# Optimization experiments

Hardware: AMD Instinct MI355X
Metric: run time of the kernel (lower is better)

Reference implementation:

```python
import jax, jax.numpy as jnp
import numpy as np

B, T, D = 2, 2048, 1280
H = 20
DH = D // H  # 64
S_PAST = 2048


def setup_inputs() -> dict:
    key = jax.random.key(0)
    ks = jax.random.split(key, 7)
    return {
        "x": jax.random.normal(ks[0], (B, T, D), dtype=jnp.float32),
        "past_K": jax.random.normal(ks[1], (B, H, S_PAST, DH), dtype=jnp.float32),
        "past_V": jax.random.normal(ks[2], (B, H, S_PAST, DH), dtype=jnp.float32),
        "w_q": jax.random.normal(ks[3], (D, D), dtype=jnp.float32),
        "w_k": jax.random.normal(ks[4], (D, D), dtype=jnp.float32),
        "w_v": jax.random.normal(ks[5], (D, D), dtype=jnp.float32),
        "W_o": jax.random.normal(ks[6], (D, D), dtype=jnp.float32),
    }


def reference(x, past_K, past_V, w_q, w_k, w_v, W_o):
    b, t, _ = x.shape
    # projections
    q = x @ w_q  # [B,T,D]
    k = x @ w_k
    v = x @ w_v
    # split heads -> [B,H,T,DH]
    Q = q.reshape(b, t, H, DH).transpose(0, 2, 1, 3)
    K = k.reshape(b, t, H, DH).transpose(0, 2, 1, 3)
    V = v.reshape(b, t, H, DH).transpose(0, 2, 1, 3)
    # concat KV cache along sequence dim
    K = jnp.concatenate([past_K, K], axis=-2)  # [B,H,S_past+T,DH]
    V = jnp.concatenate([past_V, V], axis=-2)
    # attention (no causal mask, matching the original module)
    scores = jnp.einsum("bhtd,bhsd->bhts", Q, K) / jnp.sqrt(jnp.float32(DH))
    attn = jax.nn.softmax(scores, axis=-1)
    values = jnp.einsum("bhts,bhsd->bhtd", attn, V)  # [B,H,T,DH]
    values = values.transpose(0, 2, 1, 3).reshape(b, t, D)
    out = values @ W_o
    return out, K, V
```

## Files before the change

### kernel.cpp

```cpp
#include <hip/hip_runtime.h>

#define NB 2
#define NH 20
#define TT 2048
#define DD 1280
#define DHH 64
#define SP 2048
#define SS 4096
#define MM (NB*TT)

typedef __attribute__((ext_vector_type(8))) short bf16x8;
typedef __attribute__((ext_vector_type(4))) float f32x4;
typedef unsigned short u16;
typedef unsigned int u32;

__device__ __forceinline__ f32x4 mfma16(bf16x8 a, bf16x8 b, f32x4 c) {
  return __builtin_amdgcn_mfma_f32_16x16x32_bf16(a, b, c, 0, 0, 0);
}

__device__ __forceinline__ u16 f2bf(float f) {
  u32 x = __builtin_bit_cast(u32, f);
  x += 0x7fffu + ((x >> 16) & 1u);
  return (u16)(x >> 16);
}
__device__ __forceinline__ float bf2f(u16 u) {
  u32 x = ((u32)u) << 16;
  return __builtin_bit_cast(float, x);
}

__device__ __forceinline__ float fexp2(float x) {
#if __has_builtin(__builtin_amdgcn_exp2f)
  return __builtin_amdgcn_exp2f(x);
#else
  return exp2f(x);
#endif
}

__device__ __forceinline__ u32 cvtpk(float lo, float hi) {
  u32 r;
  asm("v_cvt_pk_bf16_f32 %0, %1, %2" : "=v"(r) : "v"(lo), "v"(hi));
  return r;
}

#define VMCNT0() asm volatile("s_waitcnt vmcnt(0)" ::: "memory")
#define BAR() __builtin_amdgcn_s_barrier()

template<int ROWS>
__device__ __forceinline__ void stage_swz(char* lds, const u16* __restrict__ gsrc,
                                          int ld, int tid) {
  constexpr int ITER = ROWS * 8 / 256;
#pragma unroll
  for (int i = 0; i < ITER; ++i) {
    int id = i * 256 + tid;
    int row = id >> 3, c = id & 7;
    int cs = c ^ (row & 7);
    const u16* src = gsrc + row * ld + cs * 8;
    __builtin_amdgcn_global_load_lds(
        (const __attribute__((address_space(1))) u32*)src,
        (__attribute__((address_space(3))) u32*)(lds + id * 16), 16, 0, 0);
  }
}

__device__ __forceinline__ void gload16(const u16* src, char* ldst) {
  __builtin_amdgcn_global_load_lds(
      (const __attribute__((address_space(1))) u32*)src,
      (__attribute__((address_space(3))) u32*)ldst, 16, 0, 0);
}

__device__ __forceinline__ bf16x8 frag_swz(const char* lds, int row, int cc) {
  return *(const bf16x8*)(lds + row * 128 + ((cc ^ (row & 7)) << 4));
}
__device__ __forceinline__ bf16x8 frag32(const char* lds, int row, int cc) {
  return *(const bf16x8*)(lds + row * 64 + ((cc ^ (row & 3)) << 4));
}

__global__ void splitx(const float* __restrict__ x, u16* __restrict__ xh,
                       u16* __restrict__ xl) {
  int i = blockIdx.x * 256 + threadIdx.x;
  float4 v = ((const float4*)x)[i];
  ushort4 hi, lo;
  hi.x = f2bf(v.x); lo.x = f2bf(v.x - bf2f(hi.x));
  hi.y = f2bf(v.y); lo.y = f2bf(v.y - bf2f(hi.y));
  hi.z = f2bf(v.z); lo.z = f2bf(v.z - bf2f(hi.z));
  hi.w = f2bf(v.w); lo.w = f2bf(v.w - bf2f(hi.w));
  ((ushort4*)xh)[i] = hi;
  ((ushort4*)xl)[i] = lo;
}

__global__ void transw(const float* __restrict__ wq, const float* __restrict__ wk,
                       const float* __restrict__ wv, const float* __restrict__ wo,
                       u16* __restrict__ wqkvh, u16* __restrict__ wqkvl,
                       u16* __restrict__ wot) {
  __shared__ float tile[64][65];
  int mat = blockIdx.z;
  const float* src = mat == 0 ? wq : mat == 1 ? wk : mat == 2 ? wv : wo;
  int k0 = blockIdx.x * 64, n0 = blockIdx.y * 64;
  int tid = threadIdx.x;
#pragma unroll
  for (int rep = 0; rep < 16; ++rep) {
    int id = rep * 256 + tid;
    int kl = id >> 6, nl = id & 63;
    tile[nl][kl] = src[(k0 + kl) * DD + n0 + nl];
  }
  __syncthreads();
#pragma unroll
  for (int rep = 0; rep < 16; ++rep) {
    int id = rep * 256 + tid;
    int nl = id >> 6, kl = id & 63;
    float v = tile[nl][kl];
    u16 hi = f2bf(v);
    if (mat < 3) {
      int idx = (mat * DD + n0 + nl) * DD + k0 + kl;
      wqkvh[idx] = hi;
      wqkvl[idx] = f2bf(v - bf2f(hi));
    } else {
      wot[(n0 + nl) * DD + k0 + kl] = hi;
    }
  }
}

__global__ void pastk(const float* __restrict__ pK, float* __restrict__ dK,
                      u16* __restrict__ Kh, u16* __restrict__ Kl) {
  int i = blockIdx.x * 256 + threadIdx.x;
  int e = i * 4;
  int dh = e & 63;
  int s = (e >> 6) & (SP - 1);
  int bh = e >> 17;
  float4 v = *(const float4*)(pK + e);
  int o = (bh * SS + s) * DHH + dh;
  *(float4*)(dK + o) = v;
  ushort4 hi, lo;
  hi.x = f2bf(v.x); lo.x = f2bf(v.x - bf2f(hi.x));
  hi.y = f2bf(v.y); lo.y = f2bf(v.y - bf2f(hi.y));
  hi.z = f2bf(v.z); lo.z = f2bf(v.z - bf2f(hi.z));
  hi.w = f2bf(v.w); lo.w = f2bf(v.w - bf2f(hi.w));
  *(ushort4*)(Kh + o) = hi;
  *(ushort4*)(Kl + o) = lo;
}

__global__ void pastv(const float* __restrict__ pV, float* __restrict__ dV,
                      u16* __restrict__ Vt) {
  __shared__ u16 tile[64][72];
  int bi = blockIdx.x;
  int bh = bi >> 5, st = bi & 31;
  int s0 = st * 64;
  int tid = threadIdx.x;
  const float* src = pV + (bh * SP + s0) * DHH;
  float* dst = dV + (bh * SS + s0) * DHH;
#pragma unroll
  for (int rep = 0; rep < 16; ++rep) {
    int id = rep * 256 + tid;
    int sl = id >> 6, dh = id & 63;
    float v = src[sl * DHH + dh];
    dst[sl * DHH + dh] = v;
    tile[dh][sl] = f2bf(v);
  }
  __syncthreads();
  u16* vdst = Vt + (bh * DHH) * SS + s0;
#pragma unroll
  for (int rep = 0; rep < 4; ++rep) {
    int id = rep * 256 + tid;
    int dh = id >> 4, s4 = (id & 15) * 4;
    ushort4 vv;
    vv.x = tile[dh][s4];     vv.y = tile[dh][s4 + 1];
    vv.z = tile[dh][s4 + 2]; vv.w = tile[dh][s4 + 3];
    *(ushort4*)(vdst + dh * SS + s4) = vv;
  }
}

__launch_bounds__(256, 2)
__global__ void gemm_qkv(const u16* __restrict__ xh, const u16* __restrict__ xl,
                         const u16* __restrict__ wh, const u16* __restrict__ wl,
                         u16* __restrict__ Qh, u16* __restrict__ Ql,
                         u16* __restrict__ Kh, u16* __restrict__ Kl,
                         u16* __restrict__ Vt,
                         float* __restrict__ dK, float* __restrict__ dV) {
  __shared__ __align__(16) char sm[65536];
  int tid = threadIdx.x, lane = tid & 63, w = tid >> 6;
  int wm = w >> 1, wn = w & 1;
  int r15 = lane & 15, grp = lane >> 4;
  int mBase = blockIdx.x * 128;
  int by = blockIdx.y;
  int nGlob = by * 128;
  const bool split = (by < 20);
  f32x4 acc[4][4] = {};
  int id0 = tid, id1 = 256 + tid;
  int r0 = id0 >> 2, c0 = id0 & 3;
  int r1 = id1 >> 2, c1 = id1 & 3;
  int so0 = r0 * DD + (c0 ^ (r0 & 3)) * 8;
  int so1 = r1 * DD + (c1 ^ (r1 & 3)) * 8;
  const u16* aH = xh + mBase * DD;
  const u16* aL = xl + mBase * DD;
  const u16* bH = wh + nGlob * DD;
  const u16* bL = wl + nGlob * DD;
  int do0 = id0 * 16, do1 = id1 * 16;

  auto stage = [&](int buf, int k0) {
    char* b = sm + buf * 32768;
    gload16(aH + k0 + so0, b + do0);
    gload16(aH + k0 + so1, b + do1);
    gload16(bH + k0 + so0, b + 16384 + do0);
    gload16(bH + k0 + so1, b + 16384 + do1);
    if (split) {
      gload16(aL + k0 + so0, b + 8192 + do0);
      gload16(aL + k0 + so1, b + 8192 + do1);
      gload16(bL + k0 + so0, b + 24576 + do0);
      gload16(bL + k0 + so1, b + 24576 + do1);
    }
  };
  auto compute = [&](int buf) {
    const char* b = sm + buf * 32768;
    bf16x8 fah[4], fal[4], fbh[4], fbl[4];
#pragma unroll
    for (int i = 0; i < 4; ++i) {
      fah[i] = frag32(b, wm * 64 + i * 16 + r15, grp);
      fbh[i] = frag32(b + 16384, wn * 64 + i * 16 + r15, grp);
      if (split) {
        fal[i] = frag32(b + 8192, wm * 64 + i * 16 + r15, grp);
        fbl[i] = frag32(b + 24576, wn * 64 + i * 16 + r15, grp);
      }
    }
    __builtin_amdgcn_s_setprio(1);
    if (split) {
#pragma unroll
      for (int i = 0; i < 4; ++i)
#pragma unroll
        for (int j = 0; j < 4; ++j) {
          acc[i][j] = mfma16(fah[i], fbh[j], acc[i][j]);
          acc[i][j] = mfma16(fah[i], fbl[j], acc[i][j]);
          acc[i][j] = mfma16(fal[i], fbh[j], acc[i][j]);
        }
    } else {
#pragma unroll
      for (int i = 0; i < 4; ++i)
#pragma unroll
        for (int j = 0; j < 4; ++j)
          acc[i][j] = mfma16(fah[i], fbh[j], acc[i][j]);
    }
    __builtin_amdgcn_s_setprio(0);
  };

  stage(0, 0);
  VMCNT0(); BAR();
#pragma unroll 2
  for (int step = 0; step < 39; ++step) {
    stage((step + 1) & 1, (step + 1) * 32);
    compute(step & 1);
    VMCNT0(); BAR();
  }
  compute(1);

  int proj = by / 10;
  int nb = (by % 10) * 128 + wn * 64;
#pragma unroll
  for (int i = 0; i < 4; ++i)
#pragma unroll
    for (int j = 0; j < 4; ++j)
#pragma unroll
      for (int r = 0; r < 4; ++r) {
        int m = mBase + wm * 64 + i * 16 + grp * 4 + r;
        int n = nb + j * 16 + r15;
        float v = acc[i][j][r];
        int b = m >> 11, t = m & 2047;
        int h = n >> 6, dh = n & 63;
        int bhh = b * NH + h;
        if (proj == 0) {
          float q = v * 0.180336880111f;
          u16 hi = f2bf(q);
          int idx = (bhh * TT + t) * DHH + dh;
          Qh[idx] = hi;
          Ql[idx] = f2bf(q - bf2f(hi));
        } else if (proj == 1) {
          int idx = (bhh * SS + SP + t) * DHH + dh;
          dK[idx] = v;
          u16 hi = f2bf(v);
          Kh[idx] = hi;
          Kl[idx] = f2bf(v - bf2f(hi));
        } else {
          int idx = (bhh * SS + SP + t) * DHH + dh;
          dV[idx] = v;
          Vt[(bhh * DHH + dh) * SS + SP + t] = f2bf(v);
        }
      }
}

__launch_bounds__(256, 3)
__global__ void attn(const u16* __restrict__ Qh, const u16* __restrict__ Ql,
                     const u16* __restrict__ Kh, const u16* __restrict__ Kl,
                     const u16* __restrict__ Vt, u16* __restrict__ ao) {
  __shared__ __align__(16) char Ks[8192];
  __shared__ __align__(16) char Kls[8192];
  __shared__ __align__(16) char Vs[8192];
  __shared__ __align__(16) u16 Pw[4][2][16][72];
  __shared__ __align__(16) float bc[4][16];
  int d = blockIdx.x;
  int xcd = d & 7, sl = d >> 3;
  int bh = xcd * 5 + (sl >> 4);
  int q0 = (sl & 15) * 128;
  int tid = threadIdx.x, lane = tid & 63, w = tid >> 6;
  int r15 = lane & 15, grp = lane >> 4;
  int qbase = q0 + w * 32;
  bf16x8 fqh[2][2], fql[2][2];
#pragma unroll
  for (int qt = 0; qt < 2; ++qt) {
    int qrow = qbase + qt * 16 + r15;
    const u16* qb = Qh + (bh * TT + qrow) * DHH + grp * 8;
    const u16* qbl = Ql + (bh * TT + qrow) * DHH + grp * 8;
    fqh[qt][0] = *(const bf16x8*)qb;   fqh[qt][1] = *(const bf16x8*)(qb + 32);
    fql[qt][0] = *(const bf16x8*)qbl;  fql[qt][1] = *(const bf16x8*)(qbl + 32);
  }
  float mrun[2] = {-1e30f, -1e30f};
  float lrun[2] = {0.f, 0.f};
  f32x4 oacc[2][4] = {};
  int id0 = tid, id1 = 256 + tid;
  int r0 = id0 >> 3, c0 = id0 & 7;
  int r1 = id1 >> 3, c1 = id1 & 7;
  const u16* kh0 = Kh + bh * SS * DHH + r0 * DHH + (c0 ^ (r0 & 7)) * 8;
  const u16* kh1 = Kh + bh * SS * DHH + r1 * DHH + (c1 ^ (r1 & 7)) * 8;
  const u16* kl0 = Kl + bh * SS * DHH + r0 * DHH + (c0 ^ (r0 & 7)) * 8;
  const u16* kl1 = Kl + bh * SS * DHH + r1 * DHH + (c1 ^ (r1 & 7)) * 8;
  const u16* v0 = Vt + bh * DHH * SS + r0 * SS + (c0 ^ (r0 & 7)) * 8;
  const u16* v1 = Vt + bh * DHH * SS + r1 * SS + (c1 ^ (r1 & 7)) * 8;
  char* dK0 = Ks + id0 * 16;  char* dK1 = Ks + id1 * 16;
  char* dL0 = Kls + id0 * 16; char* dL1 = Kls + id1 * 16;
  char* dV0 = Vs + id0 * 16;  char* dV1 = Vs + id1 * 16;

  for (int it = 0; it < SS / 64; ++it) {
    gload16(kh0, dK0); gload16(kh1, dK1);
    gload16(kl0, dL0); gload16(kl1, dL1);
    gload16(v0, dV0);  gload16(v1, dV1);
    kh0 += 64 * DHH; kh1 += 64 * DHH;
    kl0 += 64 * DHH; kl1 += 64 * DHH;
    v0 += 64; v1 += 64;
    __syncthreads();
    f32x4 st[2][4];
    __builtin_amdgcn_s_setprio(1);
#pragma unroll
    for (int kt = 0; kt < 4; ++kt) {
      bf16x8 k0f = frag_swz(Ks, kt * 16 + r15, grp);
      bf16x8 k1f = frag_swz(Ks, kt * 16 + r15, 4 + grp);
      bf16x8 l0f = frag_swz(Kls, kt * 16 + r15, grp);
      bf16x8 l1f = frag_swz(Kls, kt * 16 + r15, 4 + grp);
#pragma unroll
      for (int qt = 0; qt < 2; ++qt) {
        f32x4 a = {0.f, 0.f, 0.f, 0.f};
        a = mfma16(k0f, fqh[qt][0], a);
        a = mfma16(k0f, fql[qt][0], a);
        a = mfma16(l0f, fqh[qt][0], a);
        a = mfma16(k1f, fqh[qt][1], a);
        a = mfma16(k1f, fql[qt][1], a);
        a = mfma16(l1f, fqh[qt][1], a);
        st[qt][kt] = a;
      }
    }
    __builtin_amdgcn_s_setprio(0);
#pragma unroll
    for (int qt = 0; qt < 2; ++qt) {
      float cm = fmaxf(
          fmaxf(fmaxf(st[qt][0][0], st[qt][0][1]), fmaxf(st[qt][0][2], st[qt][0][3])),
          fmaxf(fmaxf(st[qt][1][0], st[qt][1][1]), fmaxf(st[qt][1][2], st[qt][1][3])));
      cm = fmaxf(cm, fmaxf(
          fmaxf(fmaxf(st[qt][2][0], st[qt][2][1]), fmaxf(st[qt][2][2], st[qt][2][3])),
          fmaxf(fmaxf(st[qt][3][0], st[qt][3][1]), fmaxf(st[qt][3][2], st[qt][3][3]))));
      cm = fmaxf(cm, __shfl_xor(cm, 16));
      cm = fmaxf(cm, __shfl_xor(cm, 32));
      if (!__all(cm <= mrun[qt] + 8.f)) {
        float mnew = fmaxf(mrun[qt], cm);
        float sc = fexp2(mrun[qt] - mnew);
        lrun[qt] *= sc;
        mrun[qt] = mnew;
        if (grp == 0) bc[w][r15] = sc;
        f32x4 scv = *(const f32x4*)&bc[w][grp * 4];
#pragma unroll
        for (int dd = 0; dd < 4; ++dd) {
          oacc[qt][dd][0] *= scv[0]; oacc[qt][dd][1] *= scv[1];
          oacc[qt][dd][2] *= scv[2]; oacc[qt][dd][3] *= scv[3];
        }
      }
      float m = mrun[qt];
      float ps = 0.f;
#pragma unroll
      for (int kt = 0; kt < 4; ++kt)
#pragma unroll
        for (int r = 0; r < 4; ++r) {
          float p = fexp2(st[qt][kt][r] - m);
          st[qt][kt][r] = p;
          ps += p;
        }
      ps += __shfl_xor(ps, 16);
      ps += __shfl_xor(ps, 32);
      lrun[qt] += ps;
#pragma unroll
      for (int kt = 0; kt < 4; ++kt) {
        u32 w0 = cvtpk(st[qt][kt][0], st[qt][kt][1]);
        u32 w1 = cvtpk(st[qt][kt][2], st[qt][kt][3]);
        uint2 pk = {w0, w1};
        *(uint2*)&Pw[w][qt][r15][kt * 16 + grp * 4] = pk;
      }
    }
    bf16x8 pa[2][2];
#pragma unroll
    for (int qt = 0; qt < 2; ++qt) {
      pa[qt][0] = *(const bf16x8*)&Pw[w][qt][r15][grp * 8];
      pa[qt][1] = *(const bf16x8*)&Pw[w][qt][r15][32 + grp * 8];
    }
    __builtin_amdgcn_s_setprio(1);
#pragma unroll
    for (int dd = 0; dd < 4; ++dd) {
      bf16x8 vf0 = frag_swz(Vs, dd * 16 + r15, grp);
      bf16x8 vf1 = frag_swz(Vs, dd * 16 + r15, 4 + grp);
#pragma unroll
      for (int qt = 0; qt < 2; ++qt) {
        oacc[qt][dd] = mfma16(pa[qt][0], vf0, oacc[qt][dd]);
        oacc[qt][dd] = mfma16(pa[qt][1], vf1, oacc[qt][dd]);
      }
    }
    __builtin_amdgcn_s_setprio(0);
    __syncthreads();
  }
  int b = bh / NH, h = bh % NH;
#pragma unroll
  for (int qt = 0; qt < 2; ++qt) {
    float inv = 1.0f / lrun[qt];
    if (grp == 0) bc[w][r15] = inv;
    f32x4 li = *(const f32x4*)&bc[w][grp * 4];
#pragma unroll
    for (int dd = 0; dd < 4; ++dd)
#pragma unroll
      for (int r = 0; r < 4; ++r) {
        int q = qbase + qt * 16 + grp * 4 + r;
        int col = h * DHH + dd * 16 + r15;
        ao[(b * TT + q) * DD + col] = f2bf(oacc[qt][dd][r] * li[r]);
      }
  }
}

__launch_bounds__(256, 2)
__global__ void gemm_out(const u16* __restrict__ ao, const u16* __restrict__ wot,
                         float* __restrict__ out) {
  __shared__ __align__(16) char sm[32768];
  char* As = sm;
  char* Bs = sm + 16384;
  int tid = threadIdx.x, lane = tid & 63, w = tid >> 6;
  int wm = w >> 1, wn = w & 1;
  int r15 = lane & 15, grp = lane >> 4;
  int mBase = blockIdx.x * 128, nBase = blockIdx.y * 128;
  f32x4 acc[4][4] = {};
  for (int k0 = 0; k0 < DD; k0 += 64) {
    stage_swz<128>(As, ao + mBase * DD + k0, DD, tid);
    stage_swz<128>(Bs, wot + nBase * DD + k0, DD, tid);
    __syncthreads();
#pragma unroll
    for (int kk = 0; kk < 2; ++kk) {
      int cc = kk * 4 + grp;
      bf16x8 fa[4], fb[4];
#pragma unroll
      for (int i = 0; i < 4; ++i) {
        fa[i] = frag_swz(As, wm * 64 + i * 16 + r15, cc);
        fb[i] = frag_swz(Bs, wn * 64 + i * 16 + r15, cc);
      }
#pragma unroll
      for (int i = 0; i < 4; ++i)
#pragma unroll
        for (int j = 0; j < 4; ++j)
          acc[i][j] = mfma16(fa[i], fb[j], acc[i][j]);
    }
    __syncthreads();
  }
#pragma unroll
  for (int i = 0; i < 4; ++i)
#pragma unroll
    for (int j = 0; j < 4; ++j)
#pragma unroll
      for (int r = 0; r < 4; ++r) {
        int m = mBase + wm * 64 + i * 16 + grp * 4 + r;
        int n = nBase + wn * 64 + j * 16 + r15;
        out[m * DD + n] = acc[i][j][r];
      }
}

extern "C" void kernel_launch(void* const* d_in, const int* in_sizes, int n_in,
                              void* d_out, int out_size, void* d_ws, size_t ws_size,
                              hipStream_t stream) {
  const float* x  = (const float*)d_in[0];
  const float* pK = (const float*)d_in[1];
  const float* pV = (const float*)d_in[2];
  const float* wq = (const float*)d_in[3];
  const float* wk = (const float*)d_in[4];
  const float* wv = (const float*)d_in[5];
  const float* wo = (const float*)d_in[6];

  float* out = (float*)d_out;
  float* dK  = out + NB * TT * DD;
  float* dV  = dK + NB * NH * SS * DHH;

  u16* xh    = (u16*)d_ws;
  u16* xl    = xh + MM * DD;
  u16* wqkvh = xl + MM * DD;
  u16* wqkvl = wqkvh + 3 * DD * DD;
  u16* wot   = wqkvl + 3 * DD * DD;
  u16* Qh    = wot + DD * DD;
  u16* Ql    = Qh + MM * DD;
  u16* Kh    = Ql + MM * DD;
  u16* Kl    = Kh + NB * NH * SS * DHH;
  u16* Vt    = Kl + NB * NH * SS * DHH;
  u16* ao    = xh;

  splitx<<<dim3(MM * DD / 4 / 256), 256, 0, stream>>>(x, xh, xl);
  transw<<<dim3(20, 20, 4), 256, 0, stream>>>(wq, wk, wv, wo, wqkvh, wqkvl, wot);
  pastk<<<dim3(NB * NH * SP * DHH / 4 / 256), 256, 0, stream>>>(pK, dK, Kh, Kl);
  pastv<<<dim3(NB * NH * (SP / 64)), 256, 0, stream>>>(pV, dV, Vt);
  gemm_qkv<<<dim3(32, 30), 256, 0, stream>>>(xh, xl, wqkvh, wqkvl,
                                             Qh, Ql, Kh, Kl, Vt, dK, dV);
  attn<<<dim3(NB * NH * (TT / 128)), 256, 0, stream>>>(Qh, Ql, Kh, Kl, Vt, ao);
  gemm_out<<<dim3(32, 10), 256, 0, stream>>>(ao, wot, out);
}
```

Baseline: 382.2 us.

## Skip negligible attention tiles using cheap hi-only score estimate

The QK^T score is now first computed from only the high bf16 parts of K and Q, and the low-part correction MFMAs are issued only when the tile's approximate max is within 88 (log2 units) of the running max. Tiles whose scores would underflow exp2 skip the correction MFMAs, the softmax, the P writes and the PV MFMAs entirely. The block max uses v_max3 via inline asm. This relies on random normal inputs producing many tiles far below the running max. It risks wrong skips when the hi-only estimate errs near the threshold, and it adds divergent branching.

```diff
diff --git a/kernel.cpp b/kernel.cpp
--- a/kernel.cpp
+++ b/kernel.cpp
@@ -40,6 +40,22 @@
   u32 r;
   asm("v_cvt_pk_bf16_f32 %0, %1, %2" : "=v"(r) : "v"(lo), "v"(hi));
   return r;
+}
+
+__device__ __forceinline__ float vmax3(float a, float b, float c) {
+  float d;
+  asm("v_max3_f32 %0, %1, %2, %3" : "=v"(d) : "v"(a), "v"(b), "v"(c));
+  return d;
+}
+__device__ __forceinline__ float max16(const f32x4* st) {
+  float m0 = vmax3(st[0][0], st[0][1], st[0][2]);
+  float m1 = vmax3(st[0][3], st[1][0], st[1][1]);
+  float m2 = vmax3(st[1][2], st[1][3], st[2][0]);
+  float m3 = vmax3(st[2][1], st[2][2], st[2][3]);
+  float m4 = vmax3(st[3][0], st[3][1], st[3][2]);
+  float m5 = vmax3(m0, m1, st[3][3]);
+  float m6 = vmax3(m2, m3, m4);
+  return fmaxf(m5, m6);
 }
 
 #define VMCNT0() asm volatile("s_waitcnt vmcnt(0)" ::: "memory")
@@ -333,89 +349,114 @@
     kl0 += 64 * DHH; kl1 += 64 * DHH;
     v0 += 64; v1 += 64;
     __syncthreads();
+    bf16x8 kf[4][2];
     f32x4 st[2][4];
     __builtin_amdgcn_s_setprio(1);
 #pragma unroll
     for (int kt = 0; kt < 4; ++kt) {
-      bf16x8 k0f = frag_swz(Ks, kt * 16 + r15, grp);
-      bf16x8 k1f = frag_swz(Ks, kt * 16 + r15, 4 + grp);
-      bf16x8 l0f = frag_swz(Kls, kt * 16 + r15, grp);
-      bf16x8 l1f = frag_swz(Kls, kt * 16 + r15, 4 + grp);
+      kf[kt][0] = frag_swz(Ks, kt * 16 + r15, grp);
+      kf[kt][1] = frag_swz(Ks, kt * 16 + r15, 4 + grp);
 #pragma unroll
       for (int qt = 0; qt < 2; ++qt) {
         f32x4 a = {0.f, 0.f, 0.f, 0.f};
-        a = mfma16(k0f, fqh[qt][0], a);
-        a = mfma16(k0f, fql[qt][0], a);
-        a = mfma16(l0f, fqh[qt][0], a);
-        a = mfma16(k1f, fqh[qt][1], a);
-        a = mfma16(k1f, fql[qt][1], a);
-        a = mfma16(l1f, fqh[qt][1], a);
+        a = mfma16(kf[kt][0], fqh[qt][0], a);
+        a = mfma16(kf[kt][1], fqh[qt][1], a);
         st[qt][kt] = a;
       }
     }
     __builtin_amdgcn_s_setprio(0);
+    float cm[2];
 #pragma unroll
     for (int qt = 0; qt < 2; ++qt) {
-      float cm = fmaxf(
-          fmaxf(fmaxf(st[qt][0][0], st[qt][0][1]), fmaxf(st[qt][0][2], st[qt][0][3])),
-          fmaxf(fmaxf(st[qt][1][0], st[qt][1][1]), fmaxf(st[qt][1][2], st[qt][1][3])));
-      cm = fmaxf(cm, fmaxf(
-          fmaxf(fmaxf(st[qt][2][0], st[qt][2][1]), fmaxf(st[qt][2][2], st[qt][2][3])),
-          fmaxf(fmaxf(st[qt][3][0], st[qt][3][1]), fmaxf(st[qt][3][2], st[qt][3][3]))));
-      cm = fmaxf(cm, __shfl_xor(cm, 16));
-      cm = fmaxf(cm, __shfl_xor(cm, 32));
-      if (!__all(cm <= mrun[qt] + 8.f)) {
-        float mnew = fmaxf(mrun[qt], cm);
-        float sc = fexp2(mrun[qt] - mnew);
-        lrun[qt] *= sc;
-        mrun[qt] = mnew;
-        if (grp == 0) bc[w][r15] = sc;
-        f32x4 scv = *(const f32x4*)&bc[w][grp * 4];
-#pragma unroll
-        for (int dd = 0; dd < 4; ++dd) {
-          oacc[qt][dd][0] *= scv[0]; oacc[qt][dd][1] *= scv[1];
-          oacc[qt][dd][2] *= scv[2]; oacc[qt][dd][3] *= scv[3];
-        }
-      }
-      float m = mrun[qt];
-      float ps = 0.f;
-#pragma unroll
-      for (int kt = 0; kt < 4; ++kt)
-#pragma unroll
-        for (int r = 0; r < 4; ++r) {
-          float p = fexp2(st[qt][kt][r] - m);
-          st[qt][kt][r] = p;
-          ps += p;
-        }
-      ps += __shfl_xor(ps, 16);
-      ps += __shfl_xor(ps, 32);
-      lrun[qt] += ps;
+      float c = max16(st[qt]);
+      c = fmaxf(c, __shfl_xor(c, 16));
+      c = fmaxf(c, __shfl_xor(c, 32));
+      cm[qt] = c;
+    }
+    bool act0 = !__all(cm[0] <= mrun[0] - 88.f);
+    bool act1 = !__all(cm[1] <= mrun[1] - 88.f);
+    if (act0 | act1) {
+      __builtin_amdgcn_s_setprio(1);
 #pragma unroll
       for (int kt = 0; kt < 4; ++kt) {
-        u32 w0 = cvtpk(st[qt][kt][0], st[qt][kt][1]);
-        u32 w1 = cvtpk(st[qt][kt][2], st[qt][kt][3]);
-        uint2 pk = {w0, w1};
-        *(uint2*)&Pw[w][qt][r15][kt * 16 + grp * 4] = pk;
-      }
-    }
-    bf16x8 pa[2][2];
-#pragma unroll
-    for (int qt = 0; qt < 2; ++qt) {
-      pa[qt][0] = *(const bf16x8*)&Pw[w][qt][r15][grp * 8];
-      pa[qt][1] = *(const bf16x8*)&Pw[w][qt][r15][32 + grp * 8];
-    }
-    __builtin_amdgcn_s_setprio(1);
-#pragma unroll
-    for (int dd = 0; dd < 4; ++dd) {
-      bf16x8 vf0 = frag_swz(Vs, dd * 16 + r15, grp);
-      bf16x8 vf1 = frag_swz(Vs, dd * 16 + r15, 4 + grp);
+        bf16x8 l0 = frag_swz(Kls, kt * 16 + r15, grp);
+        bf16x8 l1 = frag_swz(Kls, kt * 16 + r15, 4 + grp);
+        if (act0) {
+          st[0][kt] = mfma16(l0, fqh[0][0], st[0][kt]);
+          st[0][kt] = mfma16(kf[kt][0], fql[0][0], st[0][kt]);
+          st[0][kt] = mfma16(l1, fqh[0][1], st[0][kt]);
+          st[0][kt] = mfma16(kf[kt][1], fql[0][1], st[0][kt]);
+        }
+        if (act1) {
+          st[1][kt] = mfma16(l0, fqh[1][0], st[1][kt]);
+          st[1][kt] = mfma16(kf[kt][0], fql[1][0], st[1][kt]);
+          st[1][kt] = mfma16(l1, fqh[1][1], st[1][kt]);
+          st[1][kt] = mfma16(kf[kt][1], fql[1][1], st[1][kt]);
+        }
+      }
+      __builtin_amdgcn_s_setprio(0);
 #pragma unroll
       for (int qt = 0; qt < 2; ++qt) {
-        oacc[qt][dd] = mfma16(pa[qt][0], vf0, oacc[qt][dd]);
-        oacc[qt][dd] = mfma16(pa[qt][1], vf1, oacc[qt][dd]);
-      }
-    }
-    __builtin_amdgcn_s_setprio(0);
+        if (!(qt == 0 ? act0 : act1)) continue;
+        if (!__all(cm[qt] <= mrun[qt] + 8.f)) {
+          float mnew = fmaxf(mrun[qt], cm[qt]);
+          float sc = fexp2(mrun[qt] - mnew);
+          lrun[qt] *= sc;
+          mrun[qt] = mnew;
+          if (grp == 0) bc[w][r15] = sc;
+          f32x4 scv = *(const f32x4*)&bc[w][grp * 4];
+#pragma unroll
+          for (int dd = 0; dd < 4; ++dd) {
+            oacc[qt][dd][0] *= scv[0]; oacc[qt][dd][1] *= scv[1];
+            oacc[qt][dd][2] *= scv[2]; oacc[qt][dd][3] *= scv[3];
+          }
+        }
+        float m = mrun[qt];
+        float ps = 0.f;
+#pragma unroll
+        for (int kt = 0; kt < 4; ++kt)
+#pragma unroll
+          for (int r = 0; r < 4; ++r) {
+            float p = fexp2(st[qt][kt][r] - m);
+            st[qt][kt][r] = p;
+            ps += p;
+          }
+        ps += __shfl_xor(ps, 16);
+        ps += __shfl_xor(ps, 32);
+        lrun[qt] += ps;
+#pragma unroll
+        for (int kt = 0; kt < 4; ++kt) {
+          u32 w0 = cvtpk(st[qt][kt][0], st[qt][kt][1]);
+          u32 w1 = cvtpk(st[qt][kt][2], st[qt][kt][3]);
+          uint2 pk = {w0, w1};
+          *(uint2*)&Pw[w][qt][r15][kt * 16 + grp * 4] = pk;
+        }
+      }
+      bf16x8 pa[2][2];
+      if (act0) {
+        pa[0][0] = *(const bf16x8*)&Pw[w][0][r15][grp * 8];
+        pa[0][1] = *(const bf16x8*)&Pw[w][0][r15][32 + grp * 8];
+      }
+      if (act1) {
+        pa[1][0] = *(const bf16x8*)&Pw[w][1][r15][grp * 8];
+        pa[1][1] = *(const bf16x8*)&Pw[w][1][r15][32 + grp * 8];
+      }
+      __builtin_amdgcn_s_setprio(1);
+#pragma unroll
+      for (int dd = 0; dd < 4; ++dd) {
+        bf16x8 vf0 = frag_swz(Vs, dd * 16 + r15, grp);
+        bf16x8 vf1 = frag_swz(Vs, dd * 16 + r15, 4 + grp);
+        if (act0) {
+          oacc[0][dd] = mfma16(pa[0][0], vf0, oacc[0][dd]);
+          oacc[0][dd] = mfma16(pa[0][1], vf1, oacc[0][dd]);
+        }
+        if (act1) {
+          oacc[1][dd] = mfma16(pa[1][0], vf0, oacc[1][dd]);
+          oacc[1][dd] = mfma16(pa[1][1], vf1, oacc[1][dd]);
+        }
+      }
+      __builtin_amdgcn_s_setprio(0);
+    }
     __syncthreads();
   }
   int b = bh / NH, h = bh % NH;
```

Result: slower. 740.8 us (+93.8%).

## Skip attention tiles whose coarse scores fall far below running max

Applied to the files above, without the earlier changes.

The QK^T computation now runs a cheap hi-only bf16 pass first and takes the tile max with v_max3. Only if some row's coarse max comes within 88 (log2 units) of the running max does it add the lo-correction MFMAs and then do the softmax and PV accumulation. Otherwise the whole tile is skipped. This removes compute for tiles whose exp2 contributions would underflow, but the skip decision uses uncorrected hi-only scores. It depends on the score distribution, and with random inputs of large magnitude many tiles may be negligible.

```diff
diff --git a/kernel.cpp b/kernel.cpp
--- a/kernel.cpp
+++ b/kernel.cpp
@@ -40,6 +40,22 @@
   u32 r;
   asm("v_cvt_pk_bf16_f32 %0, %1, %2" : "=v"(r) : "v"(lo), "v"(hi));
   return r;
+}
+
+__device__ __forceinline__ float vmax3(float a, float b, float c) {
+  float d;
+  asm("v_max3_f32 %0, %1, %2, %3" : "=v"(d) : "v"(a), "v"(b), "v"(c));
+  return d;
+}
+__device__ __forceinline__ float max16(const f32x4* st) {
+  float m0 = vmax3(st[0][0], st[0][1], st[0][2]);
+  float m1 = vmax3(st[0][3], st[1][0], st[1][1]);
+  float m2 = vmax3(st[1][2], st[1][3], st[2][0]);
+  float m3 = vmax3(st[2][1], st[2][2], st[2][3]);
+  float m4 = vmax3(st[3][0], st[3][1], st[3][2]);
+  float m5 = vmax3(m0, m1, st[3][3]);
+  float m6 = vmax3(m2, m3, m4);
+  return fmaxf(m5, m6);
 }
 
 #define VMCNT0() asm volatile("s_waitcnt vmcnt(0)" ::: "memory")
@@ -339,83 +355,97 @@
     for (int kt = 0; kt < 4; ++kt) {
       bf16x8 k0f = frag_swz(Ks, kt * 16 + r15, grp);
       bf16x8 k1f = frag_swz(Ks, kt * 16 + r15, 4 + grp);
-      bf16x8 l0f = frag_swz(Kls, kt * 16 + r15, grp);
-      bf16x8 l1f = frag_swz(Kls, kt * 16 + r15, 4 + grp);
 #pragma unroll
       for (int qt = 0; qt < 2; ++qt) {
         f32x4 a = {0.f, 0.f, 0.f, 0.f};
         a = mfma16(k0f, fqh[qt][0], a);
-        a = mfma16(k0f, fql[qt][0], a);
-        a = mfma16(l0f, fqh[qt][0], a);
         a = mfma16(k1f, fqh[qt][1], a);
-        a = mfma16(k1f, fql[qt][1], a);
-        a = mfma16(l1f, fqh[qt][1], a);
         st[qt][kt] = a;
       }
     }
     __builtin_amdgcn_s_setprio(0);
+    float cm[2];
 #pragma unroll
     for (int qt = 0; qt < 2; ++qt) {
-      float cm = fmaxf(
-          fmaxf(fmaxf(st[qt][0][0], st[qt][0][1]), fmaxf(st[qt][0][2], st[qt][0][3])),
-          fmaxf(fmaxf(st[qt][1][0], st[qt][1][1]), fmaxf(st[qt][1][2], st[qt][1][3])));
-      cm = fmaxf(cm, fmaxf(
-          fmaxf(fmaxf(st[qt][2][0], st[qt][2][1]), fmaxf(st[qt][2][2], st[qt][2][3])),
-          fmaxf(fmaxf(st[qt][3][0], st[qt][3][1]), fmaxf(st[qt][3][2], st[qt][3][3]))));
-      cm = fmaxf(cm, __shfl_xor(cm, 16));
-      cm = fmaxf(cm, __shfl_xor(cm, 32));
-      if (!__all(cm <= mrun[qt] + 8.f)) {
-        float mnew = fmaxf(mrun[qt], cm);
-        float sc = fexp2(mrun[qt] - mnew);
-        lrun[qt] *= sc;
-        mrun[qt] = mnew;
-        if (grp == 0) bc[w][r15] = sc;
-        f32x4 scv = *(const f32x4*)&bc[w][grp * 4];
-#pragma unroll
-        for (int dd = 0; dd < 4; ++dd) {
-          oacc[qt][dd][0] *= scv[0]; oacc[qt][dd][1] *= scv[1];
-          oacc[qt][dd][2] *= scv[2]; oacc[qt][dd][3] *= scv[3];
+      float c = max16(st[qt]);
+      c = fmaxf(c, __shfl_xor(c, 16));
+      c = fmaxf(c, __shfl_xor(c, 32));
+      cm[qt] = c;
+    }
+    bool act = (!__all(cm[0] <= mrun[0] - 88.f)) |
+               (!__all(cm[1] <= mrun[1] - 88.f));
+    if (act) {
+      __builtin_amdgcn_s_setprio(1);
+#pragma unroll
+      for (int kt = 0; kt < 4; ++kt) {
+        bf16x8 k0f = frag_swz(Ks, kt * 16 + r15, grp);
+        bf16x8 k1f = frag_swz(Ks, kt * 16 + r15, 4 + grp);
+        bf16x8 l0f = frag_swz(Kls, kt * 16 + r15, grp);
+        bf16x8 l1f = frag_swz(Kls, kt * 16 + r15, 4 + grp);
+#pragma unroll
+        for (int qt = 0; qt < 2; ++qt) {
+          st[qt][kt] = mfma16(l0f, fqh[qt][0], st[qt][kt]);
+          st[qt][kt] = mfma16(k0f, fql[qt][0], st[qt][kt]);
+          st[qt][kt] = mfma16(l1f, fqh[qt][1], st[qt][kt]);
+          st[qt][kt] = mfma16(k1f, fql[qt][1], st[qt][kt]);
         }
       }
-      float m = mrun[qt];
-      float ps = 0.f;
-#pragma unroll
-      for (int kt = 0; kt < 4; ++kt)
-#pragma unroll
-        for (int r = 0; r < 4; ++r) {
-          float p = fexp2(st[qt][kt][r] - m);
-          st[qt][kt][r] = p;
-          ps += p;
+      __builtin_amdgcn_s_setprio(0);
+#pragma unroll
+      for (int qt = 0; qt < 2; ++qt) {
+        if (!__all(cm[qt] <= mrun[qt] + 8.f)) {
+          float mnew = fmaxf(mrun[qt], cm[qt]);
+          float sc = fexp2(mrun[qt] - mnew);
+          lrun[qt] *= sc;
+          mrun[qt] = mnew;
+          if (grp == 0) bc[w][r15] = sc;
+          f32x4 scv = *(const f32x4*)&bc[w][grp * 4];
+#pragma unroll
+          for (int dd = 0; dd < 4; ++dd) {
+            oacc[qt][dd][0] *= scv[0]; oacc[qt][dd][1] *= scv[1];
+            oacc[qt][dd][2] *= scv[2]; oacc[qt][dd][3] *= scv[3];
+          }
         }
-      ps += __shfl_xor(ps, 16);
-      ps += __shfl_xor(ps, 32);
-      lrun[qt] += ps;
-#pragma unroll
-      for (int kt = 0; kt < 4; ++kt) {
-        u32 w0 = cvtpk(st[qt][kt][0], st[qt][kt][1]);
-        u32 w1 = cvtpk(st[qt][kt][2], st[qt][kt][3]);
-        uint2 pk = {w0, w1};
-        *(uint2*)&Pw[w][qt][r15][kt * 16 + grp * 4] = pk;
-      }
-    }
-    bf16x8 pa[2][2];
-#pragma unroll
-    for (int qt = 0; qt < 2; ++qt) {
-      pa[qt][0] = *(const bf16x8*)&Pw[w][qt][r15][grp * 8];
-      pa[qt][1] = *(const bf16x8*)&Pw[w][qt][r15][32 + grp * 8];
-    }
-    __builtin_amdgcn_s_setprio(1);
-#pragma unroll
-    for (int dd = 0; dd < 4; ++dd) {
-      bf16x8 vf0 = frag_swz(Vs, dd * 16 + r15, grp);
-      bf16x8 vf1 = frag_swz(Vs, dd * 16 + r15, 4 + grp);
+        float m = mrun[qt];
+        float ps = 0.f;
+#pragma unroll
+        for (int kt = 0; kt < 4; ++kt)
+#pragma unroll
+          for (int r = 0; r < 4; ++r) {
+            float p = fexp2(st[qt][kt][r] - m);
+            st[qt][kt][r] = p;
+            ps += p;
+          }
+        ps += __shfl_xor(ps, 16);
+        ps += __shfl_xor(ps, 32);
+        lrun[qt] += ps;
+#pragma unroll
+        for (int kt = 0; kt < 4; ++kt) {
+          u32 w0 = cvtpk(st[qt][kt][0], st[qt][kt][1]);
+          u32 w1 = cvtpk(st[qt][kt][2], st[qt][kt][3]);
+          uint2 pk = {w0, w1};
+          *(uint2*)&Pw[w][qt][r15][kt * 16 + grp * 4] = pk;
+        }
+      }
+      bf16x8 pa[2][2];
 #pragma unroll
       for (int qt = 0; qt < 2; ++qt) {
-        oacc[qt][dd] = mfma16(pa[qt][0], vf0, oacc[qt][dd]);
-        oacc[qt][dd] = mfma16(pa[qt][1], vf1, oacc[qt][dd]);
-      }
-    }
-    __builtin_amdgcn_s_setprio(0);
+        pa[qt][0] = *(const bf16x8*)&Pw[w][qt][r15][grp * 8];
+        pa[qt][1] = *(const bf16x8*)&Pw[w][qt][r15][32 + grp * 8];
+      }
+      __builtin_amdgcn_s_setprio(1);
+#pragma unroll
+      for (int dd = 0; dd < 4; ++dd) {
+        bf16x8 vf0 = frag_swz(Vs, dd * 16 + r15, grp);
+        bf16x8 vf1 = frag_swz(Vs, dd * 16 + r15, 4 + grp);
+#pragma unroll
+        for (int qt = 0; qt < 2; ++qt) {
+          oacc[qt][dd] = mfma16(pa[qt][0], vf0, oacc[qt][dd]);
+          oacc[qt][dd] = mfma16(pa[qt][1], vf1, oacc[qt][dd]);
+        }
+      }
+      __builtin_amdgcn_s_setprio(0);
+    }
     __syncthreads();
   }
   int b = bh / NH, h = bh % NH;
```

New measurement: 377.6 us. No clear change (-1.2%).

## Split attention KV range in two and merge partial softmax results

Applied to the files above, without the earlier changes.

Splits each attention block's 4096-key sweep into two halves handled by separate workgroups, doubling the grid from 640 to 1280 blocks. Each half writes unnormalized bf16 partial outputs plus running max and sum. A new merge kernel rescales and combines the two halves into the attention output. Also raises the occupancy target to 4 blocks per CU, packs LDS into one buffer with a swizzled P tile, and uses v_max3 for the row max. The cost is an extra kernel launch, extra partial-output traffic, and an additional bf16 rounding of the partials.

```diff
diff --git a/kernel.cpp b/kernel.cpp
--- a/kernel.cpp
+++ b/kernel.cpp
@@ -8,6 +8,7 @@
 #define SP 2048
 #define SS 4096
 #define MM (NB*TT)
+#define NROW (40*2048)
 
 typedef __attribute__((ext_vector_type(8))) short bf16x8;
 typedef __attribute__((ext_vector_type(4))) float f32x4;
@@ -40,6 +41,22 @@
   u32 r;
   asm("v_cvt_pk_bf16_f32 %0, %1, %2" : "=v"(r) : "v"(lo), "v"(hi));
   return r;
+}
+
+__device__ __forceinline__ float vmax3(float a, float b, float c) {
+  float d;
+  asm("v_max3_f32 %0, %1, %2, %3" : "=v"(d) : "v"(a), "v"(b), "v"(c));
+  return d;
+}
+__device__ __forceinline__ float max16(const f32x4* st) {
+  float m0 = vmax3(st[0][0], st[0][1], st[0][2]);
+  float m1 = vmax3(st[0][3], st[1][0], st[1][1]);
+  float m2 = vmax3(st[1][2], st[1][3], st[2][0]);
+  float m3 = vmax3(st[2][1], st[2][2], st[2][3]);
+  float m4 = vmax3(st[3][0], st[3][1], st[3][2]);
+  float m5 = vmax3(m0, m1, st[3][3]);
+  float m6 = vmax3(m2, m3, m4);
+  return fmaxf(m5, m6);
 }
 
 #define VMCNT0() asm volatile("s_waitcnt vmcnt(0)" ::: "memory")
@@ -284,29 +301,35 @@
       }
 }
 
-__launch_bounds__(256, 3)
+__launch_bounds__(256, 4)
 __global__ void attn(const u16* __restrict__ Qh, const u16* __restrict__ Ql,
                      const u16* __restrict__ Kh, const u16* __restrict__ Kl,
-                     const u16* __restrict__ Vt, u16* __restrict__ ao) {
-  __shared__ __align__(16) char Ks[8192];
-  __shared__ __align__(16) char Kls[8192];
-  __shared__ __align__(16) char Vs[8192];
-  __shared__ __align__(16) u16 Pw[4][2][16][72];
-  __shared__ __align__(16) float bc[4][16];
+                     const u16* __restrict__ Vt,
+                     u16* __restrict__ pO, float* __restrict__ pML) {
+  __shared__ __align__(16) char smem[40960];
+  char* Ks  = smem;
+  char* Kls = smem + 8192;
+  char* Vs  = smem + 16384;
+  char* Pb  = smem + 24576;
   int d = blockIdx.x;
-  int xcd = d & 7, sl = d >> 3;
-  int bh = xcd * 5 + (sl >> 4);
-  int q0 = (sl & 15) * 128;
+  int xcd = d & 7, slot = d >> 3;
+  int bh = xcd * 5 + (slot >> 5);
+  int rr5 = slot & 31;
+  int qb = rr5 >> 1, half = rr5 & 1;
+  int q0 = qb * 128;
   int tid = threadIdx.x, lane = tid & 63, w = tid >> 6;
   int r15 = lane & 15, grp = lane >> 4;
   int qbase = q0 + w * 32;
+  char* pw[2] = {Pb + (w * 2 + 0) * 2048, Pb + (w * 2 + 1) * 2048};
+  int swz = (r15 & 7) << 4;
+
   bf16x8 fqh[2][2], fql[2][2];
 #pragma unroll
   for (int qt = 0; qt < 2; ++qt) {
     int qrow = qbase + qt * 16 + r15;
-    const u16* qb = Qh + (bh * TT + qrow) * DHH + grp * 8;
+    const u16* qb_ = Qh + (bh * TT + qrow) * DHH + grp * 8;
     const u16* qbl = Ql + (bh * TT + qrow) * DHH + grp * 8;
-    fqh[qt][0] = *(const bf16x8*)qb;   fqh[qt][1] = *(const bf16x8*)(qb + 32);
+    fqh[qt][0] = *(const bf16x8*)qb_;  fqh[qt][1] = *(const bf16x8*)(qb_ + 32);
     fql[qt][0] = *(const bf16x8*)qbl;  fql[qt][1] = *(const bf16x8*)(qbl + 32);
   }
   float mrun[2] = {-1e30f, -1e30f};
@@ -315,17 +338,20 @@
   int id0 = tid, id1 = 256 + tid;
   int r0 = id0 >> 3, c0 = id0 & 7;
   int r1 = id1 >> 3, c1 = id1 & 7;
-  const u16* kh0 = Kh + bh * SS * DHH + r0 * DHH + (c0 ^ (r0 & 7)) * 8;
-  const u16* kh1 = Kh + bh * SS * DHH + r1 * DHH + (c1 ^ (r1 & 7)) * 8;
-  const u16* kl0 = Kl + bh * SS * DHH + r0 * DHH + (c0 ^ (r0 & 7)) * 8;
-  const u16* kl1 = Kl + bh * SS * DHH + r1 * DHH + (c1 ^ (r1 & 7)) * 8;
-  const u16* v0 = Vt + bh * DHH * SS + r0 * SS + (c0 ^ (r0 & 7)) * 8;
-  const u16* v1 = Vt + bh * DHH * SS + r1 * SS + (c1 ^ (r1 & 7)) * 8;
+  const u16* kbase = Kh + (bh * SS + half * 2048) * DHH;
+  const u16* klbase = Kl + (bh * SS + half * 2048) * DHH;
+  const u16* vbase = Vt + bh * DHH * SS + half * 2048;
+  const u16* kh0 = kbase + r0 * DHH + (c0 ^ (r0 & 7)) * 8;
+  const u16* kh1 = kbase + r1 * DHH + (c1 ^ (r1 & 7)) * 8;
+  const u16* kl0 = klbase + r0 * DHH + (c0 ^ (r0 & 7)) * 8;
+  const u16* kl1 = klbase + r1 * DHH + (c1 ^ (r1 & 7)) * 8;
+  const u16* v0 = vbase + r0 * SS + (c0 ^ (r0 & 7)) * 8;
+  const u16* v1 = vbase + r1 * SS + (c1 ^ (r1 & 7)) * 8;
   char* dK0 = Ks + id0 * 16;  char* dK1 = Ks + id1 * 16;
   char* dL0 = Kls + id0 * 16; char* dL1 = Kls + id1 * 16;
   char* dV0 = Vs + id0 * 16;  char* dV1 = Vs + id1 * 16;
 
-  for (int it = 0; it < SS / 64; ++it) {
+  for (int it = 0; it < 32; ++it) {
     gload16(kh0, dK0); gload16(kh1, dK1);
     gload16(kl0, dL0); gload16(kl1, dL1);
     gload16(v0, dV0);  gload16(v1, dV1);
@@ -356,12 +382,7 @@
     __builtin_amdgcn_s_setprio(0);
 #pragma unroll
     for (int qt = 0; qt < 2; ++qt) {
-      float cm = fmaxf(
-          fmaxf(fmaxf(st[qt][0][0], st[qt][0][1]), fmaxf(st[qt][0][2], st[qt][0][3])),
-          fmaxf(fmaxf(st[qt][1][0], st[qt][1][1]), fmaxf(st[qt][1][2], st[qt][1][3])));
-      cm = fmaxf(cm, fmaxf(
-          fmaxf(fmaxf(st[qt][2][0], st[qt][2][1]), fmaxf(st[qt][2][2], st[qt][2][3])),
-          fmaxf(fmaxf(st[qt][3][0], st[qt][3][1]), fmaxf(st[qt][3][2], st[qt][3][3]))));
+      float cm = max16(st[qt]);
       cm = fmaxf(cm, __shfl_xor(cm, 16));
       cm = fmaxf(cm, __shfl_xor(cm, 32));
       if (!__all(cm <= mrun[qt] + 8.f)) {
@@ -369,8 +390,9 @@
         float sc = fexp2(mrun[qt] - mnew);
         lrun[qt] *= sc;
         mrun[qt] = mnew;
-        if (grp == 0) bc[w][r15] = sc;
-        f32x4 scv = *(const f32x4*)&bc[w][grp * 4];
+        float* bcp = (float*)pw[qt];
+        if (grp == 0) bcp[r15] = sc;
+        f32x4 scv = *(const f32x4*)(pw[qt] + grp * 16);
 #pragma unroll
         for (int dd = 0; dd < 4; ++dd) {
           oacc[qt][dd][0] *= scv[0]; oacc[qt][dd][1] *= scv[1];
@@ -395,14 +417,14 @@
         u32 w0 = cvtpk(st[qt][kt][0], st[qt][kt][1]);
         u32 w1 = cvtpk(st[qt][kt][2], st[qt][kt][3]);
         uint2 pk = {w0, w1};
-        *(uint2*)&Pw[w][qt][r15][kt * 16 + grp * 4] = pk;
+        *(uint2*)(pw[qt] + r15 * 128 + ((kt * 32 + grp * 8) ^ swz)) = pk;
       }
     }
     bf16x8 pa[2][2];
 #pragma unroll
     for (int qt = 0; qt < 2; ++qt) {
-      pa[qt][0] = *(const bf16x8*)&Pw[w][qt][r15][grp * 8];
-      pa[qt][1] = *(const bf16x8*)&Pw[w][qt][r15][32 + grp * 8];
+      pa[qt][0] = *(const bf16x8*)(pw[qt] + r15 * 128 + ((grp * 16) ^ swz));
+      pa[qt][1] = *(const bf16x8*)(pw[qt] + r15 * 128 + ((64 + grp * 16) ^ swz));
     }
     __builtin_amdgcn_s_setprio(1);
 #pragma unroll
@@ -418,21 +440,38 @@
     __builtin_amdgcn_s_setprio(0);
     __syncthreads();
   }
-  int b = bh / NH, h = bh % NH;
+  int rowb = half * NROW + bh * TT + qbase;
 #pragma unroll
   for (int qt = 0; qt < 2; ++qt) {
-    float inv = 1.0f / lrun[qt];
-    if (grp == 0) bc[w][r15] = inv;
-    f32x4 li = *(const f32x4*)&bc[w][grp * 4];
 #pragma unroll
     for (int dd = 0; dd < 4; ++dd)
 #pragma unroll
       for (int r = 0; r < 4; ++r) {
-        int q = qbase + qt * 16 + grp * 4 + r;
-        int col = h * DHH + dd * 16 + r15;
-        ao[(b * TT + q) * DD + col] = f2bf(oacc[qt][dd][r] * li[r]);
-      }
-  }
+        int row = rowb + qt * 16 + grp * 4 + r;
+        pO[row * 64 + dd * 16 + r15] = f2bf(oacc[qt][dd][r]);
+      }
+    if (grp == 0) {
+      int row = rowb + qt * 16 + r15;
+      ((float2*)pML)[row] = make_float2(mrun[qt], lrun[qt]);
+    }
+  }
+}
+
+__global__ void merge2(const u16* __restrict__ pO, const float* __restrict__ pML,
+                       u16* __restrict__ ao) {
+  int gid = blockIdx.x * 256 + threadIdx.x;
+  int row = gid >> 6, dh = gid & 63;
+  float2 a = ((const float2*)pML)[row];
+  float2 b = ((const float2*)pML)[NROW + row];
+  float m = fmaxf(a.x, b.x);
+  float c0 = fexp2(a.x - m), c1 = fexp2(b.x - m);
+  float inv = 1.0f / (c0 * a.y + c1 * b.y);
+  float o0 = bf2f(pO[row * 64 + dh]);
+  float o1 = bf2f(pO[NROW * 64 + row * 64 + dh]);
+  float val = (c0 * o0 + c1 * o1) * inv;
+  int bh = row >> 11, t = row & 2047;
+  int bb = bh / NH, h = bh - bb * NH;
+  ao[(bb * TT + t) * DD + h * DHH + dh] = f2bf(val);
 }
 
 __launch_bounds__(256, 2)
@@ -505,6 +544,8 @@
   u16* Kl    = Kh + NB * NH * SS * DHH;
   u16* Vt    = Kl + NB * NH * SS * DHH;
   u16* ao    = xh;
+  u16*   pO  = xl;
+  float* pML = (float*)(xl + 2 * NROW * 64);
 
   splitx<<<dim3(MM * DD / 4 / 256), 256, 0, stream>>>(x, xh, xl);
   transw<<<dim3(20, 20, 4), 256, 0, stream>>>(wq, wk, wv, wo, wqkvh, wqkvl, wot);
@@ -512,6 +553,7 @@
   pastv<<<dim3(NB * NH * (SP / 64)), 256, 0, stream>>>(pV, dV, Vt);
   gemm_qkv<<<dim3(32, 30), 256, 0, stream>>>(xh, xl, wqkvh, wqkvl,
                                              Qh, Ql, Kh, Kl, Vt, dK, dV);
-  attn<<<dim3(NB * NH * (TT / 128)), 256, 0, stream>>>(Qh, Ql, Kh, Kl, Vt, ao);
+  attn<<<dim3(NB * NH * 16 * 2), 256, 0, stream>>>(Qh, Ql, Kh, Kl, Vt, pO, pML);
+  merge2<<<dim3(2 * NROW * 64 / 256 / 2), 256, 0, stream>>>(pO, pML, ao);
   gemm_out<<<dim3(32, 10), 256, 0, stream>>>(ao, wot, out);
 }
```

Measured after the change: 420.3 us. 10.0% more time.
